# Kernel optimization log

Hardware: AMD Instinct MI355X
Metric: run time of the kernel (lower is better)

Reference implementation:

```python
import jax, jax.numpy as jnp
import numpy as np

B, IN_DIM, FEAT_DIM, MEM_SIZE, HID, OUT_DIM = 2048, 2048, 256, 100000, 2048, 1024


def setup_inputs() -> dict:
    key = jax.random.key(0)
    ks = jax.random.split(key, 14)
    w = lambda k, shape: (jax.random.normal(k, shape, jnp.float32) * 0.02)
    return {
        "x": jax.random.normal(ks[0], (B, IN_DIM), jnp.float32),
        # feature extractor: IN_DIM -> 512 -> 256 -> FEAT_DIM
        "W1": w(ks[1], (IN_DIM, 512)), "b1": jnp.zeros((512,), jnp.float32),
        "W2": w(ks[2], (512, 256)),    "b2": jnp.zeros((256,), jnp.float32),
        "W3": w(ks[3], (256, FEAT_DIM)), "b3": jnp.zeros((FEAT_DIM,), jnp.float32),
        # external memory table
        "memory": jax.random.normal(ks[4], (MEM_SIZE, FEAT_DIM), jnp.float32),
        # task column: 2*FEAT_DIM -> HID -> HID -> OUT_DIM
        "Wt1": w(ks[5], (2 * FEAT_DIM, HID)), "bt1": jnp.zeros((HID,), jnp.float32),
        "Wt2": w(ks[6], (HID, HID)),          "bt2": jnp.zeros((HID,), jnp.float32),
        "Wo": w(ks[7], (HID, OUT_DIM)),       "bo": jnp.zeros((OUT_DIM,), jnp.float32),
    }


def reference(x, W1, b1, W2, b2, W3, b3, memory, Wt1, bt1, Wt2, bt2, Wo, bo):
    # ---- feature extractor MLP ----
    f = jax.nn.relu(x @ W1 + b1)
    f = jax.nn.relu(f @ W2 + b2)
    f = f @ W3 + b3                      # [B, FEAT_DIM]

    # ---- ExternalMemory.query ----
    # torch code detaches both features and memory before scoring (CPU/numba)
    fd = jax.lax.stop_gradient(f)
    md = jax.lax.stop_gradient(memory)
    bsz = f.shape[0]
    # scores[i] = -sum_{b,d} (f_bd - m_id)^2
    #           = -(B*||m_i||^2 - 2 m_i . sum_b f_b + sum||f||^2)
    f_sum = jnp.sum(fd, axis=0)                         # [D]
    f_sq = jnp.sum(fd * fd)                             # scalar
    m_sq = jnp.sum(md * md, axis=1)                     # [M]
    scores = -(bsz * m_sq - 2.0 * (md @ f_sum) + f_sq)  # [M]

    k = min(MEM_SIZE, bsz)  # == B here (required for the concat below)
    _, idx = jax.lax.top_k(scores, k)                   # descending, like torch.topk
    mem_out = memory[idx]                               # [B, FEAT_DIM] (grad flows to memory)

    # ---- concat + task column ----
    h = jnp.concatenate([f, mem_out], axis=-1)          # [B, 2*FEAT_DIM]
    h = jax.nn.relu(h @ Wt1 + bt1)
    h = jax.nn.relu(h @ Wt2 + bt2)
    return h @ Wo + bo                                  # [B, OUT_DIM]
```

## Files before the change

### kernel.cpp

```cpp
#include <hip/hip_runtime.h>

typedef unsigned int u32;
typedef unsigned long long u64;
typedef unsigned short u16;

typedef __attribute__((ext_vector_type(8))) short bf16x8;
typedef __attribute__((ext_vector_type(4))) float f32x4;

#define FEAT 256
#define MEMN 100000

#define OPAQ(x) asm volatile("" : "+v"(x))

static __device__ __forceinline__ u16 f2bf(float x){
  u32 u = __float_as_uint(x);
  u32 r = u + 0x7fffu + ((u >> 16) & 1u);
  return (u16)(r >> 16);
}

template<int RELU>
__global__ __launch_bounds__(256) void gemm_seq_k(const float* __restrict__ A,
                                                  const float* __restrict__ Bm,
                                                  const float* __restrict__ bias,
                                                  float* __restrict__ C,
                                                  int M, int N, int K){
  __shared__ float At[2][32][68];
  __shared__ float Bs[2][32][68];
  const int t = threadIdx.x;
  const int tx = t & 15, ty = t >> 4;
  const int bm = blockIdx.y << 6, bn = blockIdx.x << 6;
  float acc[4][4], mast[4][4];
  #pragma unroll
  for (int i = 0; i < 4; i++)
    #pragma unroll
    for (int j = 0; j < 4; j++){ acc[i][j] = 0.f; mast[i][j] = 0.f; }

  float pa[8], pb[8];
  #pragma unroll
  for (int i = 0; i < 8; i++){
    int o = t + (i << 8);
    pa[i] = A [(u64)(bm + (o >> 5)) * K + (o & 31)];
    pb[i] = Bm[(u64)(o >> 6) * N + bn + (o & 63)];
  }
  #pragma unroll
  for (int i = 0; i < 8; i++){
    int o = t + (i << 8);
    At[0][o & 31][o >> 5] = pa[i];
    Bs[0][o >> 6][o & 63] = pb[i];
  }
  __syncthreads();

  int cur = 0;
  for (int kt = 0; kt < K; kt += 32){
    const int nxt = kt + 32;
    if (nxt < K){
      #pragma unroll
      for (int i = 0; i < 8; i++){
        int o = t + (i << 8);
        pa[i] = A [(u64)(bm + (o >> 5)) * K + nxt + (o & 31)];
        pb[i] = Bm[(u64)(nxt + (o >> 6)) * N + bn + (o & 63)];
      }
    }
    #pragma unroll
    for (int k = 0; k < 32; k++){
      float4 av = *reinterpret_cast<const float4*>(&At[cur][k][ty << 2]);
      float4 bv = *reinterpret_cast<const float4*>(&Bs[cur][k][tx << 2]);
      acc[0][0] = fmaf(av.x, bv.x, acc[0][0]); acc[0][1] = fmaf(av.x, bv.y, acc[0][1]);
      acc[0][2] = fmaf(av.x, bv.z, acc[0][2]); acc[0][3] = fmaf(av.x, bv.w, acc[0][3]);
      acc[1][0] = fmaf(av.y, bv.x, acc[1][0]); acc[1][1] = fmaf(av.y, bv.y, acc[1][1]);
      acc[1][2] = fmaf(av.y, bv.z, acc[1][2]); acc[1][3] = fmaf(av.y, bv.w, acc[1][3]);
      acc[2][0] = fmaf(av.z, bv.x, acc[2][0]); acc[2][1] = fmaf(av.z, bv.y, acc[2][1]);
      acc[2][2] = fmaf(av.z, bv.z, acc[2][2]); acc[2][3] = fmaf(av.z, bv.w, acc[2][3]);
      acc[3][0] = fmaf(av.w, bv.x, acc[3][0]); acc[3][1] = fmaf(av.w, bv.y, acc[3][1]);
      acc[3][2] = fmaf(av.w, bv.z, acc[3][2]); acc[3][3] = fmaf(av.w, bv.w, acc[3][3]);
    }
    if ((nxt % 384) == 0 || nxt == K){
      #pragma unroll
      for (int i = 0; i < 4; i++)
        #pragma unroll
        for (int j = 0; j < 4; j++){ mast[i][j] = mast[i][j] + acc[i][j]; acc[i][j] = 0.f; }
    }
    if (nxt < K){
      #pragma unroll
      for (int i = 0; i < 8; i++){
        int o = t + (i << 8);
        At[cur ^ 1][o & 31][o >> 5] = pa[i];
        Bs[cur ^ 1][o >> 6][o & 63] = pb[i];
      }
      __syncthreads();
      cur ^= 1;
    }
  }
  #pragma unroll
  for (int i = 0; i < 4; i++){
    int row = bm + (ty << 2) + i;
    #pragma unroll
    for (int j = 0; j < 4; j++){
      int col = bn + (tx << 2) + j;
      float v = mast[i][j] + bias[col];
      if (RELU) v = v > 0.f ? v : 0.f;
      C[(u64)row * N + col] = v;
    }
  }
}

__global__ __launch_bounds__(64) void fsum_seq_k(const float* __restrict__ f,
                                                 float* __restrict__ fsum){
  int d = (blockIdx.x << 6) + threadIdx.x;
  float s = 0.f;
  for (int r = 0; r < 2048; r++) s += f[(u64)r * FEAT + d];
  fsum[d] = s;
}

__device__ __forceinline__ float block128_sq_avx512(const float4* base, int off, int swz){
  float e0[16], e1[16], f0[16], s16[16];
  #pragma unroll
  for (int j = 0; j < 8; j++){
    #pragma unroll
    for (int q = 0; q < 4; q++){
      float4 v = base[off + (((j << 2) + q) ^ swz)];
      float p0 = v.x * v.x, p1 = v.y * v.y, p2 = v.z * v.z, p3 = v.w * v.w;
      OPAQ(p0); OPAQ(p1); OPAQ(p2); OPAQ(p3);
      int l = q << 2;
      if (j == 0 || j == 4){ e0[l] = p0; e0[l+1] = p1; e0[l+2] = p2; e0[l+3] = p3; }
      else if (j == 1 || j == 5){ e0[l] += p0; e0[l+1] += p1; e0[l+2] += p2; e0[l+3] += p3; }
      else if (j == 2 || j == 6){ e1[l] = p0; e1[l+1] = p1; e1[l+2] = p2; e1[l+3] = p3; }
      else { e1[l] += p0; e1[l+1] += p1; e1[l+2] += p2; e1[l+3] += p3; }
    }
    if (j == 3){
      #pragma unroll
      for (int l = 0; l < 16; l++) f0[l] = e0[l] + e1[l];
    }
    if (j == 7){
      #pragma unroll
      for (int l = 0; l < 16; l++) s16[l] = f0[l] + (e0[l] + e1[l]);
    }
  }
  float h8[8], h4[4], h2[2];
  #pragma unroll
  for (int l = 0; l < 8; l++) h8[l] = s16[l] + s16[l + 8];
  #pragma unroll
  for (int l = 0; l < 4; l++) h4[l] = h8[l] + h8[l + 4];
  h2[0] = h4[0] + h4[2]; h2[1] = h4[1] + h4[3];
  return h2[0] + h2[1];
}

__global__ __launch_bounds__(256) void leaf_k(const float* __restrict__ f,
                                              float* __restrict__ lf){
  int b = blockIdx.x * 256 + threadIdx.x;
  lf[b] = block128_sq_avx512((const float4*)(f + (u64)b * 128), 0, 0);
}

__global__ __launch_bounds__(1024) void tree_k(const float* __restrict__ lf,
                                               float* __restrict__ fsq){
  __shared__ float sa[4096];
  __shared__ float sb[2048];
  int t = threadIdx.x;
  for (int i = t; i < 4096; i += 1024) sa[i] = lf[i];
  __syncthreads();
  float* src = sa; float* dst = sb;
  for (int len = 2048; len >= 1; len >>= 1){
    for (int i = t; i < len; i += 1024) dst[i] = src[2 * i] + src[2 * i + 1];
    __syncthreads();
    float* tmp = src; src = dst; dst = tmp;
  }
  if (t == 0) *fsq = src[0];
}

__global__ __launch_bounds__(256) void score_row_k(const float* __restrict__ mem,
                                                   const float* __restrict__ fsum,
                                                   const float* __restrict__ fsq_p,
                                                   u32* __restrict__ keys,
                                                   u32* __restrict__ hist,
                                                   u32* __restrict__ hist2){
  __shared__ __align__(16) float fs[256];
  __shared__ u32 lh2[256];
  const int t = threadIdx.x;
  fs[t] = fsum[t];
  lh2[t] = 0;
  __syncthreads();
  const int sub = t & 1;
  const int row = (blockIdx.x << 7) + (t >> 1);
  float key_s = 0.f; bool live = (row < MEMN);
  if (live){
    const float4* rowp = (const float4*)(mem + (u64)row * FEAT);
    const float4* s4 = (const float4*)fs;
    float dpr[4];
    #pragma unroll
    for (int j = 0; j < 4; j++) dpr[j] = 0.f;
    float msqh[2];
    #pragma unroll
    for (int blk = 0; blk < 2; blk++){
      const int off = blk << 5;
      float4 mvv[16];
      #pragma unroll
      for (int j = 0; j < 8; j++)
        #pragma unroll
        for (int cs = 0; cs < 2; cs++)
          mvv[(j << 1) | cs] = rowp[off + (j << 2) + sub + (cs << 1)];
      float e0L[8], e1L[8], f0L[8], s16L[8];
      #pragma unroll
      for (int j = 0; j < 8; j++){
        #pragma unroll
        for (int cs = 0; cs < 2; cs++){
          int kb = off + (j << 2) + sub + (cs << 1);
          float4 v = mvv[(j << 1) | cs];
          float4 fv = s4[kb];
          float p0 = v.x * v.x, p1 = v.y * v.y, p2 = v.z * v.z, p3 = v.w * v.w;
          OPAQ(p0); OPAQ(p1); OPAQ(p2); OPAQ(p3);
          int li = cs << 2;
          if (j == 0 || j == 4){ e0L[li] = p0; e0L[li+1] = p1; e0L[li+2] = p2; e0L[li+3] = p3; }
          else if (j == 1 || j == 5){ e0L[li] += p0; e0L[li+1] += p1; e0L[li+2] += p2; e0L[li+3] += p3; }
          else if (j == 2 || j == 6){ e1L[li] = p0; e1L[li+1] = p1; e1L[li+2] = p2; e1L[li+3] = p3; }
          else { e1L[li] += p0; e1L[li+1] += p1; e1L[li+2] += p2; e1L[li+3] += p3; }
          dpr[0] = fmaf(v.x, fv.x, dpr[0]);
          dpr[1] = fmaf(v.y, fv.y, dpr[1]);
          dpr[2] = fmaf(v.z, fv.z, dpr[2]);
          dpr[3] = fmaf(v.w, fv.w, dpr[3]);
        }
        if (j == 3){
          #pragma unroll
          for (int l = 0; l < 8; l++) f0L[l] = e0L[l] + e1L[l];
        }
        if (j == 7){
          #pragma unroll
          for (int l = 0; l < 8; l++) s16L[l] = f0L[l] + (e0L[l] + e1L[l]);
        }
      }
      float h8L[4], oth[4], h4v[4];
      #pragma unroll
      for (int l = 0; l < 4; l++) h8L[l] = s16L[l] + s16L[4 + l];
      #pragma unroll
      for (int l = 0; l < 4; l++) oth[l] = __shfl_xor(h8L[l], 1);
      #pragma unroll
      for (int l = 0; l < 4; l++) h4v[l] = h8L[l] + oth[l];
      float h2a = h4v[0] + h4v[2], h2b = h4v[1] + h4v[3];
      msqh[blk] = h2a + h2b;
    }
    float msq = msqh[0] + msqh[1];
    float od[4];
    #pragma unroll
    for (int i = 0; i < 4; i++) od[i] = __shfl_xor(dpr[i], 1);
    float b0 = dpr[0] + od[0], b1 = dpr[1] + od[1];
    float b2 = dpr[2] + od[2], b3 = dpr[3] + od[3];
    float dp = (b0 + b1) + (b2 + b3);
    float t1 = 2048.0f * msq;
    float t2 = 2.0f * dp;
    float d3 = t1 - t2;  OPAQ(d3);
    float d4 = d3 + fsq_p[0];
    key_s = -d4;
  }
  if (live && sub == 0){
    u32 bb = __float_as_uint(key_s);
    u32 key = (bb & 0x80000000u) ? ~bb : (bb | 0x80000000u);
    keys[row] = key;
    atomicAdd(&hist[key >> 14], 1u);
    atomicAdd(&lh2[key >> 24], 1u);
  }
  __syncthreads();
  u32 v = lh2[t];
  if (v) atomicAdd(&hist2[t], v);
}

__global__ __launch_bounds__(1024) void find_T_k(const u32* __restrict__ hist,
                                                 const u32* __restrict__ hist2,
                                                 u32* __restrict__ Tbin){
  __shared__ u32 h2[256];
  __shared__ int sh_c;
  __shared__ u32 sh_run;
  __shared__ u32 sa[1024], sb[1024];
  int t = threadIdx.x;
  if (t < 256) h2[t] = hist2[t];
  __syncthreads();
  if (t == 0){
    u32 run = 0; int cstar = 0;
    for (int c = 255; c >= 0; c--){
      u32 v = h2[c];
      if (run + v >= 2048u){ cstar = c; break; }
      run += v;
    }
    sh_c = cstar; sh_run = run;
  }
  __syncthreads();
  int cstar = sh_c; u32 run = sh_run;
  sa[t] = hist[cstar * 1024 + t];
  __syncthreads();
  u32* src = sa; u32* dst = sb;
  for (int off = 1; off < 1024; off <<= 1){
    u32 v = src[t];
    if (t + off < 1024) v += src[t + off];
    dst[t] = v;
    __syncthreads();
    u32* tmp = src; src = dst; dst = tmp;
  }
  u32 suf  = src[t];
  u32 sufn = (t < 1023) ? src[t + 1] : 0u;
  if (run + suf >= 2048u && !(run + sufn >= 2048u)) *Tbin = (u32)(cstar * 1024 + t);
}

__global__ __launch_bounds__(256) void compact_k(const u32* __restrict__ keys,
                                                 const u32* __restrict__ Tbin,
                                                 u64* __restrict__ pk,
                                                 u32* __restrict__ counter){
  int i = blockIdx.x * 256 + threadIdx.x;
  if (i >= MEMN) return;
  u32 k = keys[i];
  if ((k >> 14) >= *Tbin){
    u32 p = atomicAdd(counter, 1u);
    if (p < 4096u) pk[p] = ((u64)k << 32) | (u32)(0xFFFFFFFFu - (u32)i);
  }
}

__global__ __launch_bounds__(1024) void sort_k(const u64* __restrict__ pkin,
                                               u32* __restrict__ idxo){
  __shared__ u64 k[4096];
  for (int i = threadIdx.x; i < 4096; i += 1024) k[i] = pkin[i];
  __syncthreads();
  for (int size = 2; size <= 4096; size <<= 1){
    for (int stride = size >> 1; stride; stride >>= 1){
      #pragma unroll 2
      for (int pp = 0; pp < 2; pp++){
        int p = threadIdx.x + pp * 1024;
        int i = ((p / stride) * (stride << 1)) + (p % stride);
        int j = i + stride;
        u64 a = k[i], b = k[j];
        bool desc_ok = (a >= b);
        bool up = ((i & size) == 0);
        if (up ? !desc_ok : desc_ok){ k[i] = b; k[j] = a; }
      }
      __syncthreads();
    }
  }
  for (int i = threadIdx.x; i < 2048; i += 1024) idxo[i] = 0xFFFFFFFFu - (u32)k[i];
}

__global__ __launch_bounds__(256) void build_h_k(const float* __restrict__ f,
                                                 const float* __restrict__ mem,
                                                 const u32* __restrict__ idx,
                                                 u16* __restrict__ h){
  int r = blockIdx.x, t = threadIdx.x;
  h[(u64)r * 512 + t] = f2bf(f[(u64)r * FEAT + t]);
  h[(u64)r * 512 + 256 + t] = f2bf(mem[(u64)idx[r] * FEAT + t]);
}

__global__ void convT_k(const float* __restrict__ W, u16* __restrict__ WT, int K, int N){
  __shared__ float tile[32][33];
  int tx = threadIdx.x, ty = threadIdx.y;
  int bk = blockIdx.y << 5, bn = blockIdx.x << 5;
  #pragma unroll
  for (int i = 0; i < 4; i++){
    int r = ty + (i << 3);
    tile[r][tx] = W[(u64)(bk + r) * N + bn + tx];
  }
  __syncthreads();
  #pragma unroll
  for (int i = 0; i < 4; i++){
    int n = ty + (i << 3);
    WT[(u64)(bn + n) * K + bk + tx] = f2bf(tile[tx][n]);
  }
}

static __device__ __forceinline__ void gl_lds16(const u16* g, u16* l){
  __builtin_amdgcn_global_load_lds((const __attribute__((address_space(1))) void*)g,
                                   (__attribute__((address_space(3))) void*)l, 16, 0, 0);
}

template<int RELU, int OUTBF>
__global__ __launch_bounds__(256) void gemm_bf16_k(const u16* __restrict__ A,
                                                   const u16* __restrict__ BT,
                                                   const float* __restrict__ bias,
                                                   void* __restrict__ Cout,
                                                   int M, int N, int K){
  __shared__ u16 As[128 * 32];
  __shared__ u16 Bs[128 * 32];
  const int t = threadIdx.x;
  const int w = t >> 6, lane = t & 63;
  const int bm = blockIdx.y << 7, bn = blockIdx.x << 7;
  f32x4 acc[4][4];
  #pragma unroll
  for (int i = 0; i < 4; i++)
    #pragma unroll
    for (int j = 0; j < 4; j++) acc[i][j] = (f32x4){0.f, 0.f, 0.f, 0.f};
  const int row0 = (w >> 1) << 6, col0 = (w & 1) << 6;
  for (int kt = 0; kt < K; kt += 32){
    #pragma unroll
    for (int j = 0; j < 2; j++){
      int e = (((j << 2) + w) << 9) + (lane << 3);
      int r = e >> 5, c = e & 31;
      gl_lds16(A  + (u64)(bm + r) * K + kt + c, As + (((j << 2) + w) << 9));
      gl_lds16(BT + (u64)(bn + r) * K + kt + c, Bs + (((j << 2) + w) << 9));
    }
    __syncthreads();
    bf16x8 af[4], bfr[4];
    #pragma unroll
    for (int i = 0; i < 4; i++){
      af[i]  = *(const bf16x8*)(As + (row0 + (i << 4) + (lane & 15)) * 32 + ((lane >> 4) << 3));
      bfr[i] = *(const bf16x8*)(Bs + (col0 + (i << 4) + (lane & 15)) * 32 + ((lane >> 4) << 3));
    }
    #pragma unroll
    for (int i = 0; i < 4; i++)
      #pragma unroll
      for (int j = 0; j < 4; j++)
        acc[i][j] = __builtin_amdgcn_mfma_f32_16x16x32_bf16(af[i], bfr[j], acc[i][j], 0, 0, 0);
    __syncthreads();
  }
  #pragma unroll
  for (int i = 0; i < 4; i++){
    #pragma unroll
    for (int j = 0; j < 4; j++){
      #pragma unroll
      for (int r = 0; r < 4; r++){
        int row = bm + row0 + (i << 4) + ((lane >> 4) << 2) + r;
        int col = bn + col0 + (j << 4) + (lane & 15);
        float v = acc[i][j][r] + bias[col];
        if (RELU) v = v > 0.f ? v : 0.f;
        if (OUTBF) ((u16*)Cout)[(u64)row * N + col] = f2bf(v);
        else       ((float*)Cout)[(u64)row * N + col] = v;
      }
    }
  }
}

extern "C" void kernel_launch(void* const* d_in, const int* in_sizes, int n_in,
                              void* d_out, int out_size, void* d_ws, size_t ws_size,
                              hipStream_t stream){
  const float* x   = (const float*)d_in[0];
  const float* W1  = (const float*)d_in[1];
  const float* b1  = (const float*)d_in[2];
  const float* W2  = (const float*)d_in[3];
  const float* b2  = (const float*)d_in[4];
  const float* W3  = (const float*)d_in[5];
  const float* b3  = (const float*)d_in[6];
  const float* mem = (const float*)d_in[7];
  const float* Wt1 = (const float*)d_in[8];
  const float* bt1 = (const float*)d_in[9];
  const float* Wt2 = (const float*)d_in[10];
  const float* bt2 = (const float*)d_in[11];
  const float* Wo  = (const float*)d_in[12];
  const float* bo  = (const float*)d_in[13];

  char* ws = (char*)d_ws;
  float* f1   = (float*)(ws + 0);
  u32*   keys = (u32*)  (ws + 0);
  u32*   hist = (u32*)  (ws + 0x080000);
  u32*   hist2= (u32*)  (ws + 0x180000);
  u32*   Tbin = (u32*)  (ws + 0x180000 + 1024);
  u32*   cnt  = (u32*)  (ws + 0x180000 + 1028);
  u64*   pk   = (u64*)  (ws + 0x180000 + 4096);
  u32*   idxo = (u32*)  (ws + 0x180000 + 40960);
  float* fsum = (float*)(ws + 0x180000 + 49152);
  float* lf   = (float*)(ws + 0x180000 + 50176);
  float* fsq  = (float*)(ws + 0x180000 + 66560);
  float* f2   = (float*)(ws + (4ull  << 20));
  float* f    = (float*)(ws + (6ull  << 20));
  u16*   h    = (u16*)  (ws + (8ull  << 20));
  u16*   W1T  = (u16*)  (ws + (10ull << 20));
  u16*   W2T  = (u16*)  (ws + (12ull << 20));
  u16*   WoT  = (u16*)  (ws + (20ull << 20));
  u16*   T1   = (u16*)  (ws + (24ull << 20));
  u16*   T2   = (u16*)  (ws + (32ull << 20));

  dim3 blk(256);
  gemm_seq_k<1><<<dim3(8, 32), blk, 0, stream>>>(x,  W1, b1, f1, 2048, 512, 2048);
  gemm_seq_k<1><<<dim3(4, 32), blk, 0, stream>>>(f1, W2, b2, f2, 2048, 256, 512);
  gemm_seq_k<0><<<dim3(4, 32), blk, 0, stream>>>(f2, W3, b3, f,  2048, 256, 256);
  hipMemsetAsync(hist, 0, 1048576, stream);
  hipMemsetAsync(ws + 0x180000, 0, 36864, stream);
  fsum_seq_k <<<dim3(4),   dim3(64),   0, stream>>>(f, fsum);
  leaf_k     <<<dim3(16),  blk,        0, stream>>>(f, lf);
  tree_k     <<<dim3(1),   dim3(1024), 0, stream>>>(lf, fsq);
  score_row_k<<<dim3(782), blk,        0, stream>>>(mem, fsum, fsq, keys, hist, hist2);
  find_T_k   <<<dim3(1),   dim3(1024), 0, stream>>>(hist, hist2, Tbin);
  compact_k  <<<dim3(391), blk,        0, stream>>>(keys, Tbin, pk, cnt);
  sort_k     <<<dim3(1),   dim3(1024), 0, stream>>>(pk, idxo);
  build_h_k<<<dim3(2048), blk, 0, stream>>>(f, mem, idxo, h);
  convT_k<<<dim3(64, 16), dim3(32, 8), 0, stream>>>(Wt1, W1T, 512,  2048);
  convT_k<<<dim3(64, 64), dim3(32, 8), 0, stream>>>(Wt2, W2T, 2048, 2048);
  convT_k<<<dim3(32, 64), dim3(32, 8), 0, stream>>>(Wo,  WoT, 2048, 1024);
  gemm_bf16_k<1, 1><<<dim3(16, 16), blk, 0, stream>>>(h,  W1T, bt1, T1, 2048, 2048, 512);
  gemm_bf16_k<1, 1><<<dim3(16, 16), blk, 0, stream>>>(T1, W2T, bt2, T2, 2048, 2048, 2048);
  gemm_bf16_k<0, 0><<<dim3(8, 16),  blk, 0, stream>>>(T2, WoT, bo, (float*)d_out, 2048, 1024, 2048);
}
```

Measured before the change: 480.7 us.

## Split feature-extractor GEMMs along K into panels with a separate combine kernel

The fp32 feature-extractor GEMMs now split the K dimension into 384-wide panels, one per grid z-slice. Each slice writes its partial sums to workspace, and a combine kernel adds the partials in order, applies bias and ReLU, and writes the result. This keeps the same panel-wise summation order as the old in-block master accumulator while multiplying the number of blocks (e.g. 256 to 1536 for the first GEMM) to fill the GPU. The cost is extra global traffic for the partial buffers and three added kernel launches.

```diff
diff --git a/kernel.cpp b/kernel.cpp
--- a/kernel.cpp
+++ b/kernel.cpp
@@ -18,29 +18,31 @@
   return (u16)(r >> 16);
 }
 
-template<int RELU>
-__global__ __launch_bounds__(256) void gemm_seq_k(const float* __restrict__ A,
-                                                  const float* __restrict__ Bm,
-                                                  const float* __restrict__ bias,
-                                                  float* __restrict__ C,
-                                                  int M, int N, int K){
+__global__ __launch_bounds__(256) void gemm_panel_k(const float* __restrict__ A,
+                                                    const float* __restrict__ Bm,
+                                                    float* __restrict__ Ppart,
+                                                    int M, int N, int K){
   __shared__ float At[2][32][68];
   __shared__ float Bs[2][32][68];
   const int t = threadIdx.x;
   const int tx = t & 15, ty = t >> 4;
   const int bm = blockIdx.y << 6, bn = blockIdx.x << 6;
-  float acc[4][4], mast[4][4];
+  const int p  = blockIdx.z;
+  const int k0 = p * 384;
+  const int k1 = (k0 + 384 < K) ? (k0 + 384) : K;
+  float* Pout = Ppart + (u64)p * M * N;
+  float acc[4][4];
   #pragma unroll
   for (int i = 0; i < 4; i++)
     #pragma unroll
-    for (int j = 0; j < 4; j++){ acc[i][j] = 0.f; mast[i][j] = 0.f; }
+    for (int j = 0; j < 4; j++) acc[i][j] = 0.f;
 
   float pa[8], pb[8];
   #pragma unroll
   for (int i = 0; i < 8; i++){
     int o = t + (i << 8);
-    pa[i] = A [(u64)(bm + (o >> 5)) * K + (o & 31)];
-    pb[i] = Bm[(u64)(o >> 6) * N + bn + (o & 63)];
+    pa[i] = A [(u64)(bm + (o >> 5)) * K + k0 + (o & 31)];
+    pb[i] = Bm[(u64)(k0 + (o >> 6)) * N + bn + (o & 63)];
   }
   #pragma unroll
   for (int i = 0; i < 8; i++){
@@ -51,9 +53,9 @@
   __syncthreads();
 
   int cur = 0;
-  for (int kt = 0; kt < K; kt += 32){
+  for (int kt = k0; kt < k1; kt += 32){
     const int nxt = kt + 32;
-    if (nxt < K){
+    if (nxt < k1){
       #pragma unroll
       for (int i = 0; i < 8; i++){
         int o = t + (i << 8);
@@ -74,13 +76,7 @@
       acc[3][0] = fmaf(av.w, bv.x, acc[3][0]); acc[3][1] = fmaf(av.w, bv.y, acc[3][1]);
       acc[3][2] = fmaf(av.w, bv.z, acc[3][2]); acc[3][3] = fmaf(av.w, bv.w, acc[3][3]);
     }
-    if ((nxt % 384) == 0 || nxt == K){
-      #pragma unroll
-      for (int i = 0; i < 4; i++)
-        #pragma unroll
-        for (int j = 0; j < 4; j++){ mast[i][j] = mast[i][j] + acc[i][j]; acc[i][j] = 0.f; }
-    }
-    if (nxt < K){
+    if (nxt < k1){
       #pragma unroll
       for (int i = 0; i < 8; i++){
         int o = t + (i << 8);
@@ -97,11 +93,24 @@
     #pragma unroll
     for (int j = 0; j < 4; j++){
       int col = bn + (tx << 2) + j;
-      float v = mast[i][j] + bias[col];
-      if (RELU) v = v > 0.f ? v : 0.f;
-      C[(u64)row * N + col] = v;
-    }
-  }
+      Pout[(u64)row * N + col] = acc[i][j];
+    }
+  }
+}
+
+template<int NP, int RELU>
+__global__ __launch_bounds__(256) void combine_k(const float* __restrict__ Ppart,
+                                                 const float* __restrict__ bias,
+                                                 float* __restrict__ C,
+                                                 int N, u64 pstride){
+  u64 i = (u64)blockIdx.x * 256 + threadIdx.x;
+  float v = 0.0f + Ppart[i];
+  OPAQ(v);
+  #pragma unroll
+  for (int p = 1; p < NP; p++){ v = v + Ppart[p * pstride + i]; }
+  v = v + bias[(int)(i % (u64)N)];
+  if (RELU) v = v > 0.f ? v : 0.f;
+  C[i] = v;
 }
 
 __global__ __launch_bounds__(64) void fsum_seq_k(const float* __restrict__ f,
@@ -459,11 +468,17 @@
   u16*   WoT  = (u16*)  (ws + (20ull << 20));
   u16*   T1   = (u16*)  (ws + (24ull << 20));
   u16*   T2   = (u16*)  (ws + (32ull << 20));
+  float* Pg1  = (float*)(ws + (12ull << 20));
+  float* Pg2  = (float*)(ws + (36ull << 20));
+  float* Pg3  = (float*)(ws + (36ull << 20));
 
   dim3 blk(256);
-  gemm_seq_k<1><<<dim3(8, 32), blk, 0, stream>>>(x,  W1, b1, f1, 2048, 512, 2048);
-  gemm_seq_k<1><<<dim3(4, 32), blk, 0, stream>>>(f1, W2, b2, f2, 2048, 256, 512);
-  gemm_seq_k<0><<<dim3(4, 32), blk, 0, stream>>>(f2, W3, b3, f,  2048, 256, 256);
+  gemm_panel_k<<<dim3(8, 32, 6), blk, 0, stream>>>(x,  W1, Pg1, 2048, 512, 2048);
+  combine_k<6, 1><<<dim3(4096), blk, 0, stream>>>(Pg1, b1, f1, 512, (u64)2048 * 512);
+  gemm_panel_k<<<dim3(4, 32, 2), blk, 0, stream>>>(f1, W2, Pg2, 2048, 256, 512);
+  combine_k<2, 1><<<dim3(2048), blk, 0, stream>>>(Pg2, b2, f2, 256, (u64)2048 * 256);
+  gemm_panel_k<<<dim3(4, 32, 1), blk, 0, stream>>>(f2, W3, Pg3, 2048, 256, 256);
+  combine_k<1, 0><<<dim3(2048), blk, 0, stream>>>(Pg3, b3, f,  256, (u64)2048 * 256);
   hipMemsetAsync(hist, 0, 1048576, stream);
   hipMemsetAsync(ws + 0x180000, 0, 36864, stream);
   fsum_seq_k <<<dim3(4),   dim3(64),   0, stream>>>(f, fsum);
```

Result: faster. 459.5 us (-4.4%).
